# Performance work log

Hardware: AMD Instinct MI355X
Metric: run time of the kernel (lower is better)

The kernel has to match this reference:

```python
import jax, jax.numpy as jnp
import numpy as np

B, C, N, T = 64, 64, 325, 12


def setup_inputs() -> dict:
    key = jax.random.key(0)
    k_x, k_d, k1, k2, k3, kg = jax.random.split(key, 6)
    x = jax.random.normal(k_x, (B, C, N, T), dtype=jnp.float32)
    # positive pairwise distances (raised to real power 2*lamda3)
    dist = jax.random.uniform(k_d, (N, N), dtype=jnp.float32, minval=0.1, maxval=2.0)
    # params initialized as 2*randn-1, matching the torch module
    lamda1 = 2.0 * jax.random.normal(k1, (1,), dtype=jnp.float32) - 1.0
    lamda2 = 2.0 * jax.random.normal(k2, (1,), dtype=jnp.float32) - 1.0
    lamda3 = 2.0 * jax.random.normal(k3, (1,), dtype=jnp.float32) - 1.0
    G = 2.0 * jax.random.normal(kg, (1,), dtype=jnp.float32) - 1.0
    return {"x": x, "dist": dist, "lamda1": lamda1, "lamda2": lamda2, "lamda3": lamda3, "G": G}


def reference(x, dist, lamda1, lamda2, lamda3, G):
    b, c, n, t = x.shape
    # [B,C,N,T] -> [B*T, N, C]
    xp = jnp.transpose(x, (0, 3, 2, 1)).reshape(b * t, n, c)
    # AdaptiveAvgPool1d(2) over channel dim (c even -> mean of the two halves)
    pooled = xp.reshape(b * t, n, 2, c // 2).mean(axis=-1)   # [B*T, N, 2]
    v = jax.nn.softplus(pooled) + 1.0                          # >= 1, safe for pow
    x1 = v[..., 0]                                             # [B*T, N]
    x2 = v[..., 1]                                             # [B*T, N]
    l1 = jax.nn.softplus(lamda1)[0]
    l2 = jax.nn.softplus(lamda2)[0]
    l3 = jax.nn.softplus(lamda3)[0]
    g = jax.nn.softplus(G)[0]
    # rank-1 outer product score: pow(x1,l1) @ pow(x2,l2)^T  -> [B*T, N, N]
    dots = (x1 ** l1)[:, :, None] * (x2 ** l2)[:, None, :]
    dist2 = dist ** (2.0 * l3)                                 # [N, N], broadcasts
    inter_att = g * dots * dist2
    return jax.nn.softmax(inter_att.reshape(b, t, n, n), axis=-1)
```

## Files before the change

### kernel.cpp

```cpp
#include <hip/hip_runtime.h>
#include <math.h>

#define Bn 64
#define Cn 64
#define Nn 325
#define Tn 12
#define NT (Nn * Tn)
#define ROWS (Bn * Tn * Nn)
#define QUADS (ROWS / 4)
#define POOL_BLOCKS ((QUADS + 255) / 256)
#define DIST_BLOCKS ((Nn * Nn + 255) / 256)

__device__ __forceinline__ float sp(float x) {
    return fmaxf(x, 0.0f) + log1pf(expf(-fabsf(x)));
}

__global__ __launch_bounds__(256)
void prep_kernel(const float* __restrict__ x, const float* __restrict__ dist,
                 const float* __restrict__ l1p, const float* __restrict__ l2p,
                 const float* __restrict__ l3p,
                 float* __restrict__ x1p, float* __restrict__ x2p,
                 float* __restrict__ dist2) {
    int bid = blockIdx.x;
    if (bid < POOL_BLOCKS) {
        int q = bid * 256 + threadIdx.x;
        if (q >= QUADS) return;
        int tid0 = q * 4;
        int b = tid0 / NT;
        int r0 = tid0 - b * NT;
        const float4* p = (const float4*)(x + (size_t)b * Cn * NT + r0);
        const int cstride = NT / 4;

        float4 s1 = make_float4(0.f, 0.f, 0.f, 0.f);
        float4 s2 = make_float4(0.f, 0.f, 0.f, 0.f);
#pragma unroll
        for (int c = 0; c < 32; ++c) {
            float4 v = p[c * cstride];
            s1.x += v.x; s1.y += v.y; s1.z += v.z; s1.w += v.w;
        }
#pragma unroll
        for (int c = 32; c < 64; ++c) {
            float4 v = p[c * cstride];
            s2.x += v.x; s2.y += v.y; s2.z += v.z; s2.w += v.w;
        }

        float l1 = sp(l1p[0]);
        float l2 = sp(l2p[0]);
        float a1[4] = {s1.x, s1.y, s1.z, s1.w};
        float a2[4] = {s2.x, s2.y, s2.z, s2.w};
#pragma unroll
        for (int m = 0; m < 4; ++m) {
            int r = r0 + m;
            int n = r / Tn;
            int t = r - n * Tn;
            int o = (b * Tn + t) * Nn + n;
            float v1 = sp(a1[m] * (1.0f / 32.0f)) + 1.0f;
            float v2 = sp(a2[m] * (1.0f / 32.0f)) + 1.0f;
            x1p[o] = powf(v1, l1);
            x2p[o] = powf(v2, l2);
        }
    } else {
        int tid = (bid - POOL_BLOCKS) * 256 + threadIdx.x;
        if (tid >= Nn * Nn) return;
        float e = 2.0f * sp(l3p[0]);
        dist2[tid] = powf(dist[tid], e);
    }
}

__global__ __launch_bounds__(256)
void softmax_kernel(const float* __restrict__ x1p,
                    const float* __restrict__ x2p,
                    const float* __restrict__ dist2,
                    const float* __restrict__ Gp,
                    float* __restrict__ out) {
    int wid  = blockIdx.x * (blockDim.x >> 6) + (threadIdx.x >> 6);
    int lane = threadIdx.x & 63;
    if (wid >= ROWS) return;

    int bt = wid / Nn;
    int i  = wid - bt * Nn;

    float g   = sp(Gp[0]);
    float x1v = x1p[wid];
    const float* x2row = x2p + bt * Nn;
    const float* drow  = dist2 + i * Nn;

    float a[6];
    float m = -INFINITY;
#pragma unroll
    for (int k = 0; k < 6; ++k) {
        int j = lane + 64 * k;
        float av = -INFINITY;
        if (j < Nn) av = (g * (x1v * x2row[j])) * drow[j];
        a[k] = av;
        m = fmaxf(m, av);
    }
#pragma unroll
    for (int off = 32; off; off >>= 1) m = fmaxf(m, __shfl_xor(m, off, 64));

    float s = 0.0f;
#pragma unroll
    for (int k = 0; k < 6; ++k) {
        int j = lane + 64 * k;
        float e = 0.0f;
        if (j < Nn) e = expf(a[k] - m);
        a[k] = e;
        s += e;
    }
#pragma unroll
    for (int off = 32; off; off >>= 1) s += __shfl_xor(s, off, 64);

    float inv = 1.0f / s;
    float* orow = out + (size_t)wid * Nn;
#pragma unroll
    for (int k = 0; k < 6; ++k) {
        int j = lane + 64 * k;
        if (j < Nn) __builtin_nontemporal_store(a[k] * inv, orow + j);
    }
}

extern "C" void kernel_launch(void* const* d_in, const int* in_sizes, int n_in,
                              void* d_out, int out_size, void* d_ws, size_t ws_size,
                              hipStream_t stream) {
    const float* x    = (const float*)d_in[0];
    const float* dist = (const float*)d_in[1];
    const float* l1   = (const float*)d_in[2];
    const float* l2   = (const float*)d_in[3];
    const float* l3   = (const float*)d_in[4];
    const float* G    = (const float*)d_in[5];
    float* out = (float*)d_out;

    float* ws    = (float*)d_ws;
    float* x1p   = ws;
    float* x2p   = ws + ROWS;
    float* dist2 = ws + 2 * ROWS;

    prep_kernel<<<POOL_BLOCKS + DIST_BLOCKS, 256, 0, stream>>>(
        x, dist, l1, l2, l3, x1p, x2p, dist2);
    softmax_kernel<<<ROWS / 4, 256, 0, stream>>>(x1p, x2p, dist2, G, out);
}
```

Before: 411.4 us.

## Stage softmax rows in LDS and write contiguous float4 output

```diff
diff --git a/kernel.cpp b/kernel.cpp
--- a/kernel.cpp
+++ b/kernel.cpp
@@ -10,6 +10,12 @@
 #define QUADS (ROWS / 4)
 #define POOL_BLOCKS ((QUADS + 255) / 256)
 #define DIST_BLOCKS ((Nn * Nn + 255) / 256)
+
+#define RPB 16
+#define SMX_BLOCKS (ROWS / RPB)
+#define STAGE4 (RPB * Nn / 4)
+
+typedef float f32x4 __attribute__((ext_vector_type(4)));
 
 __device__ __forceinline__ float sp(float x) {
     return fmaxf(x, 0.0f) + log1pf(expf(-fabsf(x)));
@@ -73,49 +79,74 @@
                     const float* __restrict__ dist2,
                     const float* __restrict__ Gp,
                     float* __restrict__ out) {
-    int wid  = blockIdx.x * (blockDim.x >> 6) + (threadIdx.x >> 6);
-    int lane = threadIdx.x & 63;
-    if (wid >= ROWS) return;
+    __shared__ __align__(16) float stage[RPB * Nn];
+    __shared__ float x2s[2][Nn];
 
-    int bt = wid / Nn;
-    int i  = wid - bt * Nn;
+    const int tid  = threadIdx.x;
+    const int wave = tid >> 6;
+    const int lane = tid & 63;
+    const int wid0 = blockIdx.x * RPB;
 
-    float g   = sp(Gp[0]);
-    float x1v = x1p[wid];
-    const float* x2row = x2p + bt * Nn;
-    const float* drow  = dist2 + i * Nn;
+    const int bt0 = wid0 / Nn;
+    const int btL = (wid0 + RPB - 1) / Nn;
 
-    float a[6];
-    float m = -INFINITY;
+    for (int j = tid; j < Nn; j += 256) x2s[0][j] = x2p[bt0 * Nn + j];
+    if (btL != bt0) {
+        for (int j = tid; j < Nn; j += 256) x2s[1][j] = x2p[btL * Nn + j];
+    }
+    __syncthreads();
+
+    const float g = sp(Gp[0]);
+
+    for (int r = wave * 4; r < wave * 4 + 4; ++r) {
+        const int wid = wid0 + r;
+        const int bt  = wid / Nn;
+        const int i   = wid - bt * Nn;
+        const float* x2row = x2s[bt != bt0 ? 1 : 0];
+        const float* drow  = dist2 + i * Nn;
+        const float s1 = g * x1p[wid];
+
+        float p[6];
+        float m = -INFINITY;
 #pragma unroll
-    for (int k = 0; k < 6; ++k) {
-        int j = lane + 64 * k;
-        float av = -INFINITY;
-        if (j < Nn) av = (g * (x1v * x2row[j])) * drow[j];
-        a[k] = av;
-        m = fmaxf(m, av);
+        for (int k = 0; k < 6; ++k) {
+            int j = lane + 64 * k;
+            float pv = -INFINITY;
+            if (j < Nn) pv = x2row[j] * drow[j];
+            p[k] = pv;
+            m = fmaxf(m, pv);
+        }
+#pragma unroll
+        for (int off = 32; off; off >>= 1) m = fmaxf(m, __shfl_xor(m, off, 64));
+
+        float s = 0.0f;
+#pragma unroll
+        for (int k = 0; k < 6; ++k) {
+            int j = lane + 64 * k;
+            float e = 0.0f;
+            if (j < Nn) e = expf((p[k] - m) * s1);
+            p[k] = e;
+            s += e;
+        }
+#pragma unroll
+        for (int off = 32; off; off >>= 1) s += __shfl_xor(s, off, 64);
+
+        const float inv = 1.0f / s;
+        float* srow = stage + r * Nn;
+#pragma unroll
+        for (int k = 0; k < 6; ++k) {
+            int j = lane + 64 * k;
+            if (j < Nn) srow[j] = p[k] * inv;
+        }
     }
+    __syncthreads();
+
+    const f32x4* src = (const f32x4*)stage;
+    f32x4* dst = (f32x4*)(out + (size_t)wid0 * Nn);
 #pragma unroll
-    for (int off = 32; off; off >>= 1) m = fmaxf(m, __shfl_xor(m, off, 64));
-
-    float s = 0.0f;
-#pragma unroll
-    for (int k = 0; k < 6; ++k) {
-        int j = lane + 64 * k;
-        float e = 0.0f;
-        if (j < Nn) e = expf(a[k] - m);
-        a[k] = e;
-        s += e;
-    }
-#pragma unroll
-    for (int off = 32; off; off >>= 1) s += __shfl_xor(s, off, 64);
-
-    float inv = 1.0f / s;
-    float* orow = out + (size_t)wid * Nn;
-#pragma unroll
-    for (int k = 0; k < 6; ++k) {
-        int j = lane + 64 * k;
-        if (j < Nn) __builtin_nontemporal_store(a[k] * inv, orow + j);
+    for (int it = 0; it < (STAGE4 + 255) / 256; ++it) {
+        int idx = it * 256 + tid;
+        if (idx < STAGE4) __builtin_nontemporal_store(src[idx], dst + idx);
     }
 }
 
@@ -137,5 +168,5 @@
 
     prep_kernel<<<POOL_BLOCKS + DIST_BLOCKS, 256, 0, stream>>>(
         x, dist, l1, l2, l3, x1p, x2p, dist2);
-    softmax_kernel<<<ROWS / 4, 256, 0, stream>>>(x1p, x2p, dist2, G, out);
+    softmax_kernel<<<SMX_BLOCKS, 256, 0, stream>>>(x1p, x2p, dist2, G, out);
 }
```

Result: faster. 396.8 us (-3.5%).

## Process four softmax rows per wave, reuse x2 row, use exp2 with factored scale

Applied to the files above, without the earlier changes.

```diff
diff --git a/kernel.cpp b/kernel.cpp
--- a/kernel.cpp
+++ b/kernel.cpp
@@ -10,6 +10,11 @@
 #define QUADS (ROWS / 4)
 #define POOL_BLOCKS ((QUADS + 255) / 256)
 #define DIST_BLOCKS ((Nn * Nn + 255) / 256)
+
+#define RPB 16
+#define CHUNKS ((Nn + RPB - 1) / RPB)
+#define SMX_BLOCKS (Bn * Tn * CHUNKS)
+#define LOG2E 1.4426950408889634f
 
 __device__ __forceinline__ float sp(float x) {
     return fmaxf(x, 0.0f) + log1pf(expf(-fabsf(x)));
@@ -73,49 +78,80 @@
                     const float* __restrict__ dist2,
                     const float* __restrict__ Gp,
                     float* __restrict__ out) {
-    int wid  = blockIdx.x * (blockDim.x >> 6) + (threadIdx.x >> 6);
-    int lane = threadIdx.x & 63;
-    if (wid >= ROWS) return;
+    const int bid   = blockIdx.x;
+    const int bt    = bid / CHUNKS;
+    const int chunk = bid - bt * CHUNKS;
+    const int i0    = chunk * RPB;
+    const int wave  = threadIdx.x >> 6;
+    const int lane  = threadIdx.x & 63;
+    const int iw    = i0 + wave * 4;
 
-    int bt = wid / Nn;
-    int i  = wid - bt * Nn;
+    const float g = sp(Gp[0]);
+    const float* x2row = x2p + bt * Nn;
+    const float* x1row = x1p + bt * Nn;
 
-    float g   = sp(Gp[0]);
-    float x1v = x1p[wid];
-    const float* x2row = x2p + bt * Nn;
-    const float* drow  = dist2 + i * Nn;
-
-    float a[6];
-    float m = -INFINITY;
+    float x2r[6];
 #pragma unroll
     for (int k = 0; k < 6; ++k) {
         int j = lane + 64 * k;
-        float av = -INFINITY;
-        if (j < Nn) av = (g * (x1v * x2row[j])) * drow[j];
-        a[k] = av;
-        m = fmaxf(m, av);
+        x2r[k] = (j < Nn) ? x2row[j] : 0.0f;
+    }
+
+    float p[4][6];
+    float mx[4], sum[4], s1e[4];
+
+#pragma unroll
+    for (int r = 0; r < 4; ++r) {
+        int ic = min(iw + r, Nn - 1);
+        const float* drow = dist2 + ic * Nn;
+        float m = -INFINITY;
+#pragma unroll
+        for (int k = 0; k < 6; ++k) {
+            int j = lane + 64 * k;
+            float pv = -INFINITY;
+            if (j < Nn) pv = x2r[k] * drow[j];
+            p[r][k] = pv;
+            m = fmaxf(m, pv);
+        }
+        mx[r] = m;
+        s1e[r] = g * x1row[ic] * LOG2E;
     }
 #pragma unroll
-    for (int off = 32; off; off >>= 1) m = fmaxf(m, __shfl_xor(m, off, 64));
+    for (int off = 32; off; off >>= 1) {
+#pragma unroll
+        for (int r = 0; r < 4; ++r) mx[r] = fmaxf(mx[r], __shfl_xor(mx[r], off, 64));
+    }
 
-    float s = 0.0f;
 #pragma unroll
-    for (int k = 0; k < 6; ++k) {
-        int j = lane + 64 * k;
-        float e = 0.0f;
-        if (j < Nn) e = expf(a[k] - m);
-        a[k] = e;
-        s += e;
+    for (int r = 0; r < 4; ++r) {
+        float bshift = -mx[r] * s1e[r];
+        float s = 0.0f;
+#pragma unroll
+        for (int k = 0; k < 6; ++k) {
+            float e = exp2f(fmaf(p[r][k], s1e[r], bshift));
+            p[r][k] = e;
+            s += e;
+        }
+        sum[r] = s;
     }
 #pragma unroll
-    for (int off = 32; off; off >>= 1) s += __shfl_xor(s, off, 64);
+    for (int off = 32; off; off >>= 1) {
+#pragma unroll
+        for (int r = 0; r < 4; ++r) sum[r] += __shfl_xor(sum[r], off, 64);
+    }
 
-    float inv = 1.0f / s;
-    float* orow = out + (size_t)wid * Nn;
 #pragma unroll
-    for (int k = 0; k < 6; ++k) {
-        int j = lane + 64 * k;
-        if (j < Nn) __builtin_nontemporal_store(a[k] * inv, orow + j);
+    for (int r = 0; r < 4; ++r) {
+        int i = iw + r;
+        if (i < Nn) {
+            float inv = 1.0f / sum[r];
+            float* orow = out + ((size_t)bt * Nn + i) * (size_t)Nn;
+#pragma unroll
+            for (int k = 0; k < 6; ++k) {
+                int j = lane + 64 * k;
+                if (j < Nn) __builtin_nontemporal_store(p[r][k] * inv, orow + j);
+            }
+        }
     }
 }
 
@@ -137,5 +173,5 @@
 
     prep_kernel<<<POOL_BLOCKS + DIST_BLOCKS, 256, 0, stream>>>(
         x, dist, l1, l2, l3, x1p, x2p, dist2);
-    softmax_kernel<<<ROWS / 4, 256, 0, stream>>>(x1p, x2p, dist2, G, out);
+    softmax_kernel<<<SMX_BLOCKS, 256, 0, stream>>>(x1p, x2p, dist2, G, out);
 }
```

New measurement: 396.6 us. -3.6%, faster.
